# Kernel tuning notes

Hardware: AMD Instinct MI355X
Metric: run time of the kernel (lower is better)

The kernel has to match this reference:

```python
import jax, jax.numpy as jnp
import numpy as np

B, S, D, H, L, V = 2, 512, 1024, 16, 12, 50257
HD = D // H
DFF = 4 * D


def _ln(x, g, b, eps=1e-5):
    m = jnp.mean(x, axis=-1, keepdims=True)
    v = jnp.var(x, axis=-1, keepdims=True)
    return (x - m) * jax.lax.rsqrt(v + eps) * g + b


def setup_inputs() -> dict:
    key = jax.random.key(0)
    ks = jax.random.split(key, 32)
    sc = 0.02
    n = lambda k, shape: (jax.random.normal(k, shape, dtype=jnp.float32) * sc)
    inp = {
        "input_ids": jax.random.randint(ks[0], (B, S), 0, V, dtype=jnp.int64),
        "attention_mask": jnp.ones((B, S), dtype=jnp.float32),
        "image_hidden_states": jax.random.normal(ks[1], (B, D), dtype=jnp.float32),
        # token embedding table (also used for position embeds and tied lm_head, as in source)
        "wte": n(ks[2], (V, D)),
        # feature_space_transformation_nn: Linear(1024,1024) -> ReLU -> Linear(1024,1024)
        "ft_W1": n(ks[3], (D, D)), "ft_b1": jnp.zeros((D,), jnp.float32),
        "ft_W2": n(ks[4], (D, D)), "ft_b2": jnp.zeros((D,), jnp.float32),
        # per-layer params, stacked on leading L dim
        "ln1_g": jnp.ones((L, D), jnp.float32), "ln1_b": jnp.zeros((L, D), jnp.float32),
        "Wattn": n(ks[5], (L, D, 3 * D)), "battn": jnp.zeros((L, 3 * D), jnp.float32),
        "Wuk": n(ks[6], (L, D, D)), "buk": jnp.zeros((L, D), jnp.float32),
        "Wuv": n(ks[7], (L, D, D)), "buv": jnp.zeros((L, D), jnp.float32),
        "Wproj": n(ks[8], (L, D, D)), "bproj": jnp.zeros((L, D), jnp.float32),
        "ln2_g": jnp.ones((L, D), jnp.float32), "ln2_b": jnp.zeros((L, D), jnp.float32),
        "Wfc": n(ks[9], (L, D, DFF)), "bfc": jnp.zeros((L, DFF), jnp.float32),
        "Wfc2": n(ks[10], (L, DFF, D)), "bfc2": jnp.zeros((L, D), jnp.float32),
        "lnf_g": jnp.ones((D,), jnp.float32), "lnf_b": jnp.zeros((D,), jnp.float32),
    }
    return inp


def _forward(input_ids, attention_mask, image_hidden_states, wte,
             ft_W1, ft_b1, ft_W2, ft_b2,
             ln1_g, ln1_b, Wattn, battn, Wuk, buk, Wuv, buv, Wproj, bproj,
             ln2_g, ln2_b, Wfc, bfc, Wfc2, bfc2, lnf_g, lnf_b):
    # image feature transformation: Linear -> ReLU -> Linear
    img = jax.nn.relu(image_hidden_states @ ft_W1 + ft_b1) @ ft_W2 + ft_b2  # [B,D]

    # NOTE: source uses wte (not wpe) for position embeddings — faithful reproduction
    h = wte[input_ids] + wte[jnp.arange(S)][None]  # [B,S,D]

    # extended attention mask with a prepended zero column for the image token
    mask_ext = (1.0 - attention_mask)[:, None, None, :] * -10000.0  # [B,1,1,S]
    mask_ext = jnp.concatenate([jnp.zeros((B, 1, 1, 1), mask_ext.dtype), mask_ext], axis=-1)  # [B,1,1,S+1]

    # causal mask over kv_len=S+1: query i sees keys j <= i+1 (image token always visible)
    causal = jnp.arange(S + 1)[None, :] <= (jnp.arange(S)[:, None] + 1)  # [S,S+1]

    def block(h, p):
        (l1g, l1b, Wa, ba, Wk, bk, Wv, bv, Wp, bp, l2g, l2b, Wf, bf, Wf2, bf2) = p
        x = _ln(h, l1g, l1b)
        qkv = x @ Wa + ba
        q, k, v = jnp.split(qkv, 3, axis=-1)  # each [B,S,D]
        ki = (img @ Wk + bk)[:, None, :]  # [B,1,D]
        vi = (img @ Wv + bv)[:, None, :]
        k = jnp.concatenate([ki, k], axis=1)  # [B,S+1,D]
        v = jnp.concatenate([vi, v], axis=1)
        sh = lambda t, n: t.reshape(B, n, H, HD).transpose(0, 2, 1, 3)
        qh, kh, vh = sh(q, S), sh(k, S + 1), sh(v, S + 1)
        s = jnp.einsum('bhqd,bhkd->bhqk', qh, kh) / jnp.sqrt(jnp.float32(HD))
        s = jnp.where(causal[None, None], s, jnp.float32(-10000.0))
        s = s + mask_ext
        a = jax.nn.softmax(s, axis=-1)
        o = jnp.einsum('bhqk,bhkd->bhqd', a, vh).transpose(0, 2, 1, 3).reshape(B, S, D)
        h = h + (o @ Wp + bp)
        x = _ln(h, l2g, l2b)
        h = h + (jax.nn.gelu(x @ Wf + bf, approximate=True) @ Wf2 + bf2)
        return h, None

    params = (ln1_g, ln1_b, Wattn, battn, Wuk, buk, Wuv, buv, Wproj, bproj,
              ln2_g, ln2_b, Wfc, bfc, Wfc2, bfc2)
    h, _ = jax.lax.scan(block, h, params)
    h = _ln(h, lnf_g, lnf_b)
    return h @ wte.T  # tied lm head -> [B,S,V]


def reference(input_ids, attention_mask, image_hidden_states, wte,
              ft_W1, ft_b1, ft_W2, ft_b2,
              ln1_g, ln1_b, Wattn, battn, Wuk, buk, Wuv, buv, Wproj, bproj,
              ln2_g, ln2_b, Wfc, bfc, Wfc2, bfc2, lnf_g, lnf_b):
    return _forward(input_ids, attention_mask, image_hidden_states, wte,
                    ft_W1, ft_b1, ft_W2, ft_b2,
                    ln1_g, ln1_b, Wattn, battn, Wuk, buk, Wuv, buv, Wproj, bproj,
                    ln2_g, ln2_b, Wfc, bfc, Wfc2, bfc2, lnf_g, lnf_b)
```

## Files before the change

kernel.cpp:

```cpp
#include <hip/hip_runtime.h>
#include <cstdint>


typedef __bf16 bf16x8 __attribute__((ext_vector_type(8)));
typedef __bf16 bf16x4 __attribute__((ext_vector_type(4)));
typedef float  f32x4  __attribute__((ext_vector_type(4)));

#define GLDS16(g, l) __builtin_amdgcn_global_load_lds( \
    (const __attribute__((address_space(1))) unsigned int*)(g), \
    (__attribute__((address_space(3))) unsigned int*)(l), 16, 0, 0)

#define SCHED_FENCE() __builtin_amdgcn_sched_barrier(0)

__device__ __forceinline__ float gelu_f(float x) {
    float u = 1.5957691216057308f * (x + 0.044715f * x * x * x);
    float e = __expf(u);
    float t = 1.0f - 2.0f / (e + 1.0f);
    return 0.5f * x * (1.0f + t);
}

__device__ __forceinline__ int fragoff(int row, int kh, int hi) {
    return row * 64 + ((kh * 32 + hi * 8) ^ ((row & 7) << 3));
}

__device__ __forceinline__ void tcvt_body(
    int id, const float* __restrict__ Wa, const float* __restrict__ Wp,
    const float* __restrict__ Wf, const float* __restrict__ Wf2,
    __bf16* __restrict__ oa, __bf16* __restrict__ op,
    __bf16* __restrict__ of, __bf16* __restrict__ of2, float* tile)
{
    const float* src; __bf16* dst; int K, N, kb, nb;
    if (id < 768)       { src = Wa;  dst = oa;  K = 1024; N = 3072; kb = id & 15; nb = id >> 4; }
    else if (id < 1024) { id -= 768;  src = Wp;  dst = op;  K = 1024; N = 1024; kb = id & 15; nb = id >> 4; }
    else if (id < 2048) { id -= 1024; src = Wf;  dst = of;  K = 1024; N = 4096; kb = id & 15; nb = id >> 4; }
    else                { id -= 2048; src = Wf2; dst = of2; K = 4096; N = 1024; kb = id & 63; nb = id >> 6; }
    const int k0 = kb * 64, n0 = nb * 64;
    const int t = threadIdx.x;
    #pragma unroll
    for (int i = 0; i < 4; i++) {
        int r = i * 16 + (t >> 4), c = (t & 15) * 4;
        float4 v = *reinterpret_cast<const float4*>(src + (long)(k0 + r) * N + n0 + c);
        tile[r * 65 + c] = v.x; tile[r * 65 + c + 1] = v.y;
        tile[r * 65 + c + 2] = v.z; tile[r * 65 + c + 3] = v.w;
    }
    __syncthreads();
    const int nrow = t >> 2, kc = (t & 3) * 16;
    bf16x8 o0, o1;
    #pragma unroll
    for (int i = 0; i < 8; i++) {
        o0[i] = (__bf16)tile[(kc + i) * 65 + nrow];
        o1[i] = (__bf16)tile[(kc + 8 + i) * 65 + nrow];
    }
    *reinterpret_cast<bf16x8*>(dst + (long)(n0 + nrow) * K + k0 + kc)     = o0;
    *reinterpret_cast<bf16x8*>(dst + (long)(n0 + nrow) * K + k0 + kc + 8) = o1;
}

__device__ __forceinline__ void wcvt_body(
    int id, const float* __restrict__ wte, __bf16* __restrict__ out, long nvalid)
{
    long base = (long)id * 8192 + threadIdx.x * 8;
    #pragma unroll
    for (int i = 0; i < 4; i++) {
        long e = base + (long)i * 2048;
        bf16x8 o;
        if (e < nvalid) {
            float4 a = *reinterpret_cast<const float4*>(wte + e);
            float4 b = *reinterpret_cast<const float4*>(wte + e + 4);
            o[0] = (__bf16)a.x; o[1] = (__bf16)a.y; o[2] = (__bf16)a.z; o[3] = (__bf16)a.w;
            o[4] = (__bf16)b.x; o[5] = (__bf16)b.y; o[6] = (__bf16)b.z; o[7] = (__bf16)b.w;
        } else {
            #pragma unroll
            for (int q = 0; q < 8; q++) o[q] = (__bf16)0.f;
        }
        *reinterpret_cast<bf16x8*>(out + e) = o;
    }
}

__global__ __launch_bounds__(256) void tcvt_std(
    const float* __restrict__ Wa, const float* __restrict__ Wp,
    const float* __restrict__ Wf, const float* __restrict__ Wf2,
    __bf16* __restrict__ oa, __bf16* __restrict__ op,
    __bf16* __restrict__ of, __bf16* __restrict__ of2)
{
    __shared__ float tile[64 * 65];
    tcvt_body(blockIdx.x, Wa, Wp, Wf, Wf2, oa, op, of, of2, tile);
}

__global__ __launch_bounds__(256) void wcvt_std(
    const float* __restrict__ wte, __bf16* __restrict__ out, long nvalid)
{
    wcvt_body(blockIdx.x, wte, out, nvalid);
}

__global__ __launch_bounds__(256) void gemv_part(
    const float* __restrict__ x, int xld,
    const float* __restrict__ W, long wzs,
    float* __restrict__ part, int K, int N)
{
    int jb = blockIdx.x, kz = blockIdx.y, z = blockIdx.z;
    int t = threadIdx.x;
    int j = (jb << 6) + (t & 63);
    int g = t >> 6;
    int klen = K / (gridDim.y * 4);
    int kbase = (kz * 4 + g) * klen;
    const float* Wp = W + (long)z * wzs + (long)kbase * N + j;
    const float* x0 = x + kbase;
    const float* x1 = x + xld + kbase;
    float a0 = 0.f, a1 = 0.f;
    for (int k = 0; k < klen; k++) {
        float wv = Wp[(long)k * N];
        a0 += x0[k] * wv;
        a1 += x1[k] * wv;
    }
    __shared__ float r0[4][64], r1[4][64];
    r0[g][t & 63] = a0; r1[g][t & 63] = a1;
    __syncthreads();
    if (t < 64) {
        a0 = r0[0][t] + r0[1][t] + r0[2][t] + r0[3][t];
        a1 = r1[0][t] + r1[1][t] + r1[2][t] + r1[3][t];
        long base = (long)(z * gridDim.y + kz) * 2 * N + (jb << 6) + t;
        part[base]     = a0;
        part[base + N] = a1;
    }
}

__global__ __launch_bounds__(256) void gemv_reduce(
    const float* __restrict__ part, const float* __restrict__ bias, long bzs,
    float* __restrict__ out, int N, int nz, int act)
{
    int idx = blockIdx.x * 256 + threadIdx.x;
    if (idx >= nz * 2 * N) return;
    int j  = idx % N;
    int bz = idx / N;
    int z  = bz >> 1;
    float s = bias[(long)z * bzs + j];
    const float* p = part + ((long)z * 8 * 2 + (bz & 1)) * N + j;
    #pragma unroll
    for (int kz = 0; kz < 8; kz++) s += p[(long)kz * 2 * N];
    if (act) s = fmaxf(s, 0.f);
    out[idx] = s;
}

__global__ __launch_bounds__(256) void gemv_kv_part(
    const float* __restrict__ img,
    const float* __restrict__ Wuk, const float* __restrict__ Wuv,
    float* __restrict__ part)
{
    int jb = blockIdx.x, kz = blockIdx.y, z = blockIdx.z;
    int t = threadIdx.x;
    int j = (jb << 6) + (t & 63);
    int g = t >> 6;
    int kbase = (kz * 4 + g) * 64;
    const float* W = (z < 12) ? (Wuk + (long)z * 1048576) : (Wuv + (long)(z - 12) * 1048576);
    const float* Wp = W + (long)kbase * 1024 + j;
    const float* x0 = img + kbase;
    const float* x1 = img + 1024 + kbase;
    float a0 = 0.f, a1 = 0.f;
    for (int k = 0; k < 64; k++) {
        float wv = Wp[(long)k * 1024];
        a0 += x0[k] * wv;
        a1 += x1[k] * wv;
    }
    __shared__ float r0[4][64], r1[4][64];
    r0[g][t & 63] = a0; r1[g][t & 63] = a1;
    __syncthreads();
    if (t < 64) {
        a0 = r0[0][t] + r0[1][t] + r0[2][t] + r0[3][t];
        a1 = r1[0][t] + r1[1][t] + r1[2][t] + r1[3][t];
        long base = (long)(z * 4 + kz) * 2 * 1024 + (jb << 6) + t;
        part[base]        = a0;
        part[base + 1024] = a1;
    }
}

__global__ __launch_bounds__(256) void gemv_kv_reduce(
    const float* __restrict__ part,
    const float* __restrict__ buk, const float* __restrict__ buv,
    float* __restrict__ imgk, float* __restrict__ imgv)
{
    int idx = blockIdx.x * 256 + threadIdx.x;
    int z = idx >> 11;
    int bsel = (idx >> 10) & 1;
    int j = idx & 1023;
    float s = (z < 12) ? buk[z * 1024 + j] : buv[(z - 12) * 1024 + j];
    const float* p = part + ((long)z * 4 * 2 + bsel) * 1024 + j;
    #pragma unroll
    for (int kz = 0; kz < 4; kz++) s += p[(long)kz * 2 * 1024];
    if (z < 12) imgk[z * 2048 + bsel * 1024 + j] = s;
    else        imgv[(z - 12) * 2048 + bsel * 1024 + j] = s;
}

__global__ __launch_bounds__(256) void embed_ln(
    const int* __restrict__ ids, const float* __restrict__ wte,
    float* __restrict__ h, __bf16* __restrict__ xb,
    const float* __restrict__ g, const float* __restrict__ b)
{
    int row = blockIdx.x;
    int s = row & 511;
    int t = threadIdx.x;
    long id = ids[row];
    float4 v1 = reinterpret_cast<const float4*>(wte + id * 1024)[t];
    float4 v2 = reinterpret_cast<const float4*>(wte + (long)s * 1024)[t];
    float4 v; v.x = v1.x + v2.x; v.y = v1.y + v2.y; v.z = v1.z + v2.z; v.w = v1.w + v2.w;
    reinterpret_cast<float4*>(h + (long)row * 1024)[t] = v;

    float s1 = v.x + v.y + v.z + v.w;
    float s2 = v.x * v.x + v.y * v.y + v.z * v.z + v.w * v.w;
    #pragma unroll
    for (int o = 32; o >= 1; o >>= 1) { s1 += __shfl_xor(s1, o); s2 += __shfl_xor(s2, o); }
    __shared__ float r1[4], r2[4];
    int w = t >> 6;
    if ((t & 63) == 0) { r1[w] = s1; r2[w] = s2; }
    __syncthreads();
    s1 = r1[0] + r1[1] + r1[2] + r1[3];
    s2 = r2[0] + r2[1] + r2[2] + r2[3];
    float mean = s1 * (1.0f / 1024.0f);
    float var  = s2 * (1.0f / 1024.0f) - mean * mean;
    float rstd = rsqrtf(var + 1e-5f);
    float4 gg = reinterpret_cast<const float4*>(g)[t];
    float4 bb = reinterpret_cast<const float4*>(b)[t];
    bf16x4 o;
    o[0] = (__bf16)((v.x - mean) * rstd * gg.x + bb.x);
    o[1] = (__bf16)((v.y - mean) * rstd * gg.y + bb.y);
    o[2] = (__bf16)((v.z - mean) * rstd * gg.z + bb.z);
    o[3] = (__bf16)((v.w - mean) * rstd * gg.w + bb.w);
    *reinterpret_cast<bf16x4*>(xb + (long)row * 1024 + t * 4) = o;
}

__global__ __launch_bounds__(256) void ln_k(
    const float* __restrict__ in, __bf16* __restrict__ out,
    const float* __restrict__ g, const float* __restrict__ b)
{
    int row = blockIdx.x, t = threadIdx.x;
    float4 v = reinterpret_cast<const float4*>(in + (long)row * 1024)[t];
    float s1 = v.x + v.y + v.z + v.w;
    float s2 = v.x * v.x + v.y * v.y + v.z * v.z + v.w * v.w;
    #pragma unroll
    for (int o = 32; o >= 1; o >>= 1) { s1 += __shfl_xor(s1, o); s2 += __shfl_xor(s2, o); }
    __shared__ float r1[4], r2[4];
    int w = t >> 6;
    if ((t & 63) == 0) { r1[w] = s1; r2[w] = s2; }
    __syncthreads();
    s1 = r1[0] + r1[1] + r1[2] + r1[3];
    s2 = r2[0] + r2[1] + r2[2] + r2[3];
    float mean = s1 * (1.0f / 1024.0f);
    float var  = s2 * (1.0f / 1024.0f) - mean * mean;
    float rstd = rsqrtf(var + 1e-5f);
    float4 gg = reinterpret_cast<const float4*>(g)[t];
    float4 bb = reinterpret_cast<const float4*>(b)[t];
    bf16x4 o;
    o[0] = (__bf16)((v.x - mean) * rstd * gg.x + bb.x);
    o[1] = (__bf16)((v.y - mean) * rstd * gg.y + bb.y);
    o[2] = (__bf16)((v.z - mean) * rstd * gg.z + bb.z);
    o[3] = (__bf16)((v.w - mean) * rstd * gg.w + bb.w);
    *reinterpret_cast<bf16x4*>(out + (long)row * 1024 + t * 4) = o;
}

template<int NP>
__global__ __launch_bounds__(256) void lnadd_k(
    float* __restrict__ h, const float* __restrict__ part,
    const float* __restrict__ bias,
    const float* __restrict__ g, const float* __restrict__ b,
    __bf16* __restrict__ out)
{
    int row = blockIdx.x, t = threadIdx.x;
    long off = (long)row * 1024 + t * 4;
    float4 v = *reinterpret_cast<const float4*>(h + off);
    #pragma unroll
    for (int sp = 0; sp < NP; sp++) {
        float4 pv = *reinterpret_cast<const float4*>(part + sp * 1048576L + off);
        v.x += pv.x; v.y += pv.y; v.z += pv.z; v.w += pv.w;
    }
    float4 bi = reinterpret_cast<const float4*>(bias)[t];
    v.x += bi.x; v.y += bi.y; v.z += bi.z; v.w += bi.w;
    *reinterpret_cast<float4*>(h + off) = v;

    float s1 = v.x + v.y + v.z + v.w;
    float s2 = v.x * v.x + v.y * v.y + v.z * v.z + v.w * v.w;
    #pragma unroll
    for (int o = 32; o >= 1; o >>= 1) { s1 += __shfl_xor(s1, o); s2 += __shfl_xor(s2, o); }
    __shared__ float r1[4], r2[4];
    int w = t >> 6;
    if ((t & 63) == 0) { r1[w] = s1; r2[w] = s2; }
    __syncthreads();
    s1 = r1[0] + r1[1] + r1[2] + r1[3];
    s2 = r2[0] + r2[1] + r2[2] + r2[3];
    float mean = s1 * (1.0f / 1024.0f);
    float var  = s2 * (1.0f / 1024.0f) - mean * mean;
    float rstd = rsqrtf(var + 1e-5f);
    float4 gg = reinterpret_cast<const float4*>(g)[t];
    float4 bb = reinterpret_cast<const float4*>(b)[t];
    bf16x4 o;
    o[0] = (__bf16)((v.x - mean) * rstd * gg.x + bb.x);
    o[1] = (__bf16)((v.y - mean) * rstd * gg.y + bb.y);
    o[2] = (__bf16)((v.z - mean) * rstd * gg.z + bb.z);
    o[3] = (__bf16)((v.w - mean) * rstd * gg.w + bb.w);
    *reinterpret_cast<bf16x4*>(out + off) = o;
}

__global__ __launch_bounds__(512) void gemm256(
    const __bf16* __restrict__ A, const __bf16* __restrict__ Bt,
    float* __restrict__ C, int N, int K, int GM, int GN)
{
    const int total = GM * GN;
    const int q = total >> 3, r = total & 7;
    const int x = blockIdx.x & 7, jj = blockIdx.x >> 3;
    const int w0 = (x < r) ? x * (q + 1) + jj : r * (q + 1) + (x - r) * q + jj;
    const int m0 = (w0 % GM) * 256;
    const int n0 = (w0 / GM) * 256;

    __shared__ __bf16 As[2][256 * 64];
    __shared__ __bf16 Bs[2][256 * 64];
    const int t = threadIdx.x;
    const int wid = t >> 6, lane = t & 63;
    const int lo = lane & 15, hi = lane >> 4;
    const int wr = wid >> 2, wc = wid & 3;

    f32x4 acc[8][4] = {};

    const int srow = t >> 3;
    const int skx  = (((t & 7) ^ (srow & 7)) << 3);
    const int sldst = t * 8;
    #define ST256(bf, kk) do { \
        _Pragma("unroll") \
        for (int i = 0; i < 4; i++) \
            GLDS16(A + (long)(m0 + i * 64 + srow) * K + (kk) + skx, &As[bf][i * 4096 + sldst]); \
        _Pragma("unroll") \
        for (int i = 0; i < 4; i++) \
            GLDS16(Bt + (long)(n0 + i * 64 + srow) * K + (kk) + skx, &Bs[bf][i * 4096 + sldst]); \
    } while (0)

    const int T = K >> 6;
    ST256(0, 0);
    int cur = 0;
    for (int it = 0; it < T; it++) {
        if (it + 1 < T) {
            ST256(cur ^ 1, (it + 1) * 64);
            asm volatile("s_waitcnt vmcnt(8)" ::: "memory");
        } else {
            asm volatile("s_waitcnt vmcnt(0)" ::: "memory");
        }
        SCHED_FENCE();
        __builtin_amdgcn_s_barrier();
        SCHED_FENCE();

        #pragma unroll
        for (int kh = 0; kh < 2; kh++) {
            bf16x8 afr[8], bfr[4];
            #pragma unroll
            for (int mi = 0; mi < 8; mi++)
                afr[mi] = *reinterpret_cast<const bf16x8*>(&As[cur][fragoff(wr * 128 + mi * 16 + lo, kh, hi)]);
            #pragma unroll
            for (int ni = 0; ni < 4; ni++)
                bfr[ni] = *reinterpret_cast<const bf16x8*>(&Bs[cur][fragoff(wc * 64 + ni * 16 + lo, kh, hi)]);
            #pragma unroll
            for (int mi = 0; mi < 8; mi++)
                #pragma unroll
                for (int ni = 0; ni < 4; ni++)
                    acc[mi][ni] = __builtin_amdgcn_mfma_f32_16x16x32_bf16(afr[mi], bfr[ni], acc[mi][ni], 0, 0, 0);
        }

        SCHED_FENCE();
        __builtin_amdgcn_s_barrier();
        SCHED_FENCE();
        cur ^= 1;
    }
    #undef ST256

    #pragma unroll
    for (int mi = 0; mi < 8; mi++)
        #pragma unroll
        for (int ni = 0; ni < 4; ni++) {
            int col = n0 + wc * 64 + ni * 16 + lo;
            if (col >= N) continue;
            #pragma unroll
            for (int rr = 0; rr < 4; rr++) {
                int row = m0 + wr * 128 + mi * 16 + hi * 4 + rr;
                C[(long)row * N + col] = acc[mi][ni][rr];
            }
        }
}

template<int BN, int OUTBF16, int ACT, int PARTIAL>
__global__ __launch_bounds__(256) void gemm64(
    const __bf16* __restrict__ A, const __bf16* __restrict__ Bt,
    const float* __restrict__ bias, void* __restrict__ C,
    int N, int K, int GM, int GN, int NS)
{
    constexpr int NB = BN / 32;
    const int total = GM * GN * NS;
    const int q = total >> 3, r = total & 7;
    const int x = blockIdx.x & 7, jj = blockIdx.x >> 3;
    const int w0 = (x < r) ? x * (q + 1) + jj : r * (q + 1) + (x - r) * q + jj;
    const int sp = w0 / (GM * GN);
    const int rem = w0 - sp * (GM * GN);
    const int m0 = (rem % GM) * 64;
    const int n0 = (rem / GM) * BN;

    __shared__ __bf16 As[2][64 * 64];
    __shared__ __bf16 Bs[2][BN * 64];
    const int t = threadIdx.x;
    const int wv = t >> 6, lane = t & 63;
    const int lo = lane & 15, hi = lane >> 4;
    const int wr = wv >> 1, wc = wv & 1;

    f32x4 acc[2][NB] = {};

    const int srow = t >> 3;
    const int skx  = (((t & 7) ^ (srow & 7)) << 3);
    const int sldst = t * 8;
    #define ST64(bf, kk) do { \
        _Pragma("unroll") \
        for (int i = 0; i < 2; i++) \
            GLDS16(A + (long)(m0 + i * 32 + srow) * K + (kk) + skx, &As[bf][i * 2048 + sldst]); \
        _Pragma("unroll") \
        for (int i = 0; i < NB; i++) \
            GLDS16(Bt + (long)(n0 + i * 32 + srow) * K + (kk) + skx, &Bs[bf][i * 2048 + sldst]); \
    } while (0)

    const int Ksp = K / NS;
    const int kbeg = sp * Ksp;
    const int T = Ksp >> 6;

    ST64(0, kbeg);
    int cur = 0;
    for (int it = 0; it < T; it++) {
        if (it + 1 < T) {
            ST64(cur ^ 1, kbeg + (it + 1) * 64);
            if constexpr (NB == 4) asm volatile("s_waitcnt vmcnt(6)" ::: "memory");
            else                   asm volatile("s_waitcnt vmcnt(4)" ::: "memory");
        } else {
            asm volatile("s_waitcnt vmcnt(0)" ::: "memory");
        }
        SCHED_FENCE();
        __builtin_amdgcn_s_barrier();
        SCHED_FENCE();

        #pragma unroll
        for (int kh = 0; kh < 2; kh++) {
            bf16x8 afr[2], bfr[NB];
            #pragma unroll
            for (int mi = 0; mi < 2; mi++)
                afr[mi] = *reinterpret_cast<const bf16x8*>(&As[cur][fragoff(wr * 32 + mi * 16 + lo, kh, hi)]);
            #pragma unroll
            for (int ni = 0; ni < NB; ni++)
                bfr[ni] = *reinterpret_cast<const bf16x8*>(&Bs[cur][fragoff(wc * (BN / 2) + ni * 16 + lo, kh, hi)]);
            #pragma unroll
            for (int mi = 0; mi < 2; mi++)
                #pragma unroll
                for (int ni = 0; ni < NB; ni++)
                    acc[mi][ni] = __builtin_amdgcn_mfma_f32_16x16x32_bf16(afr[mi], bfr[ni], acc[mi][ni], 0, 0, 0);
        }

        SCHED_FENCE();
        __builtin_amdgcn_s_barrier();
        SCHED_FENCE();
        cur ^= 1;
    }
    #undef ST64

    const long coff = PARTIAL ? (long)sp * GM * 64 * N : 0;
    #pragma unroll
    for (int mi = 0; mi < 2; mi++)
        #pragma unroll
        for (int ni = 0; ni < NB; ni++) {
            int col = n0 + wc * (BN / 2) + ni * 16 + lo;
            float bv = (!PARTIAL && bias) ? bias[col] : 0.f;
            #pragma unroll
            for (int rr = 0; rr < 4; rr++) {
                int row = m0 + wr * 32 + mi * 16 + hi * 4 + rr;
                float v = acc[mi][ni][rr] + bv;
                if (ACT) v = gelu_f(v);
                if (OUTBF16) ((__bf16*)C)[(long)row * N + col] = (__bf16)v;
                else         ((float*)C)[coff + (long)row * N + col] = v;
            }
        }
}

template<int OUTBF16, int ACT, int RES>
__global__ __launch_bounds__(256) void gemm_bb(
    const __bf16* __restrict__ A, const __bf16* __restrict__ Bt,
    const float* __restrict__ bias, const float* __restrict__ res,
    void* __restrict__ C, int N, int K)
{
    __shared__ __bf16 As[64 * 32];
    __shared__ __bf16 Bs[64 * 32];
    const int t = threadIdx.x;
    const int m0 = blockIdx.x * 64;
    const int n0 = blockIdx.y * 64;
    const int w = t >> 6, lane = t & 63;
    const int lo = lane & 15, hi = lane >> 4;
    const int wr = w >> 1, wc = w & 1;

    f32x4 acc[2][2] = {};

    for (int k0 = 0; k0 < K; k0 += 32) {
        __syncthreads();
        GLDS16(A  + (long)(m0 + (t >> 2)) * K + k0 + ((t & 3) << 3), &As[t * 8]);
        GLDS16(Bt + (long)(n0 + (t >> 2)) * K + k0 + ((t & 3) << 3), &Bs[t * 8]);
        __syncthreads();
        bf16x8 afr[2], bfr[2];
        #pragma unroll
        for (int mi = 0; mi < 2; mi++)
            afr[mi] = *reinterpret_cast<const bf16x8*>(&As[(wr * 32 + mi * 16 + lo) * 32 + hi * 8]);
        #pragma unroll
        for (int ni = 0; ni < 2; ni++)
            bfr[ni] = *reinterpret_cast<const bf16x8*>(&Bs[(wc * 32 + ni * 16 + lo) * 32 + hi * 8]);
        #pragma unroll
        for (int mi = 0; mi < 2; mi++)
            #pragma unroll
            for (int ni = 0; ni < 2; ni++)
                acc[mi][ni] = __builtin_amdgcn_mfma_f32_16x16x32_bf16(afr[mi], bfr[ni], acc[mi][ni], 0, 0, 0);
    }

    #pragma unroll
    for (int mi = 0; mi < 2; mi++)
        #pragma unroll
        for (int ni = 0; ni < 2; ni++) {
            int col = n0 + wc * 32 + ni * 16 + lo;
            float bv = bias ? bias[col] : 0.f;
            #pragma unroll
            for (int rr = 0; rr < 4; rr++) {
                int row = m0 + wr * 32 + mi * 16 + hi * 4 + rr;
                float v = acc[mi][ni][rr] + bv;
                if (ACT) v = gelu_f(v);
                if (RES) v += res[(long)row * N + col];
                if (OUTBF16) ((__bf16*)C)[(long)row * N + col] = (__bf16)v;
                else         ((float*)C)[(long)row * N + col] = v;
            }
        }
}

__global__ __launch_bounds__(256) void gemm_lm(
    const __bf16* __restrict__ A, const float* __restrict__ Wt,
    float* __restrict__ C, int N, int K)
{
    __shared__ __bf16 As[128 * 32];
    __shared__ __bf16 Bs[128 * 32];
    const int t = threadIdx.x;
    const int m0 = blockIdx.x * 128;
    const int n0 = blockIdx.y * 128;
    const int w = t >> 6, lane = t & 63;
    const int lo = lane & 15, hi = lane >> 4;
    const int wr = w >> 1, wc = w & 1;

    f32x4 acc[4][4] = {};

    for (int k0 = 0; k0 < K; k0 += 32) {
        __syncthreads();
        #pragma unroll
        for (int i = 0; i < 2; i++) {
            int c = i * 256 + t;
            GLDS16(A + (long)(m0 + (c >> 2)) * K + k0 + ((c & 3) << 3), &As[c * 8]);
        }
        #pragma unroll
        for (int i = 0; i < 2; i++) {
            int c = i * 256 + t;
            int nr = n0 + (c >> 2);
            bf16x8 bv;
            if (nr < N) {
                const float* wp = Wt + (long)nr * K + k0 + ((c & 3) << 3);
                float4 b0 = *reinterpret_cast<const float4*>(wp);
                float4 b1 = *reinterpret_cast<const float4*>(wp + 4);
                bv[0] = (__bf16)b0.x; bv[1] = (__bf16)b0.y; bv[2] = (__bf16)b0.z; bv[3] = (__bf16)b0.w;
                bv[4] = (__bf16)b1.x; bv[5] = (__bf16)b1.y; bv[6] = (__bf16)b1.z; bv[7] = (__bf16)b1.w;
            } else {
                #pragma unroll
                for (int qq = 0; qq < 8; qq++) bv[qq] = (__bf16)0.f;
            }
            *reinterpret_cast<bf16x8*>(&Bs[c * 8]) = bv;
        }
        __syncthreads();
        bf16x8 afr[4], bfr[4];
        #pragma unroll
        for (int mi = 0; mi < 4; mi++)
            afr[mi] = *reinterpret_cast<const bf16x8*>(&As[(wr * 64 + mi * 16 + lo) * 32 + hi * 8]);
        #pragma unroll
        for (int ni = 0; ni < 4; ni++)
            bfr[ni] = *reinterpret_cast<const bf16x8*>(&Bs[(wc * 64 + ni * 16 + lo) * 32 + hi * 8]);
        #pragma unroll
        for (int mi = 0; mi < 4; mi++)
            #pragma unroll
            for (int ni = 0; ni < 4; ni++)
                acc[mi][ni] = __builtin_amdgcn_mfma_f32_16x16x32_bf16(afr[mi], bfr[ni], acc[mi][ni], 0, 0, 0);
    }

    #pragma unroll
    for (int mi = 0; mi < 4; mi++)
        #pragma unroll
        for (int ni = 0; ni < 4; ni++) {
            int col = n0 + wc * 64 + ni * 16 + lo;
            if (col < N) {
                #pragma unroll
                for (int rr = 0; rr < 4; rr++) {
                    int row = m0 + wr * 64 + mi * 16 + hi * 4 + rr;
                    C[(long)row * N + col] = acc[mi][ni][rr];
                }
            }
        }
}

__global__ __launch_bounds__(256) void attn_aux(
    const __bf16* __restrict__ qkv,
    const float* __restrict__ imgk, const float* __restrict__ imgv,
    const float* __restrict__ amask, __bf16* __restrict__ out,
    int aux_mode,
    const float* __restrict__ Wa, const float* __restrict__ Wp,
    const float* __restrict__ Wf, const float* __restrict__ Wf2,
    __bf16* __restrict__ oa, __bf16* __restrict__ op,
    __bf16* __restrict__ of, __bf16* __restrict__ of2,
    const float* __restrict__ wte, __bf16* __restrict__ wteb, long nvalid)
{
    __shared__ __align__(16) char smem[28416];
    const int bid = blockIdx.x;
    if (bid >= 256) {
        if (aux_mode == 1)
            tcvt_body(bid - 256, Wa, Wp, Wf, Wf2, oa, op, of, of2, (float*)smem);
        else
            wcvt_body(bid - 256, wte, wteb, nvalid);
        return;
    }

    __bf16 (*Ks)[72] = (__bf16(*)[72])(smem);
    __bf16 (*Vt)[72] = (__bf16(*)[72])(smem + 9216);
    __bf16 (*Ps)[16][72] = (__bf16(*)[16][72])(smem + 18432);
    float* kimg_s = (float*)(smem + 27648);
    float* amv_s  = (float*)(smem + 27904);

    const int qb = bid & 7;
    const int h  = (bid >> 3) & 15;
    const int b  = bid >> 7;
    const int t = threadIdx.x, w = t >> 6, lane = t & 63;
    const int lo = lane & 15, hi = lane >> 4;

    const int kr8 = t >> 2, kd8 = (t & 3) * 16;
    const int vr8 = t & 63, vd8 = (t >> 6) * 16;

    const __bf16* qrow = qkv + (long)(b * 512 + qb * 64 + w * 16 + lo) * 3072 + h * 64;
    bf16x8 qf0 = *reinterpret_cast<const bf16x8*>(qrow + hi * 8);
    bf16x8 qf1 = *reinterpret_cast<const bf16x8*>(qrow + 32 + hi * 8);

    if (t < 64) kimg_s[t] = imgk[b * 1024 + h * 64 + t];
    __syncthreads();

    float simg = 0.f;
    #pragma unroll
    for (int i = 0; i < 8; i++)
        simg += (float)qf0[i] * kimg_s[hi * 8 + i] + (float)qf1[i] * kimg_s[32 + hi * 8 + i];
    simg += __shfl_xor(simg, 16);
    simg += __shfl_xor(simg, 32);
    simg *= 0.125f;

    float pimg[4], l_part[4];
    f32x4 o_acc[4];
    #pragma unroll
    for (int rr = 0; rr < 4; rr++) {
        pimg[rr] = __expf(__shfl(simg, hi * 4 + rr));
        l_part[rr] = 0.f;
    }
    #pragma unroll
    for (int df = 0; df < 4; df++) {
        float vi = imgv[b * 1024 + h * 64 + df * 16 + lo];
        #pragma unroll
        for (int rr = 0; rr < 4; rr++) o_acc[df][rr] = pimg[rr] * vi;
    }

    bf16x8 ck0, ck1, cv0, cv1;
    {
        const __bf16* ks = qkv + (long)(b * 512 + kr8) * 3072 + 1024 + h * 64 + kd8;
        ck0 = *reinterpret_cast<const bf16x8*>(ks);
        ck1 = *reinterpret_cast<const bf16x8*>(ks + 8);
        const __bf16* vs = qkv + (long)(b * 512 + vr8) * 3072 + 2048 + h * 64 + vd8;
        cv0 = *reinterpret_cast<const bf16x8*>(vs);
        cv1 = *reinterpret_cast<const bf16x8*>(vs + 8);
    }

    for (int kb = 0; kb <= qb; kb++) {
        bf16x8 nk0, nk1, nv0, nv1;
        const bool more = (kb < qb);
        if (more) {
            const __bf16* ks = qkv + (long)(b * 512 + (kb + 1) * 64 + kr8) * 3072 + 1024 + h * 64 + kd8;
            nk0 = *reinterpret_cast<const bf16x8*>(ks);
            nk1 = *reinterpret_cast<const bf16x8*>(ks + 8);
            const __bf16* vs = qkv + (long)(b * 512 + (kb + 1) * 64 + vr8) * 3072 + 2048 + h * 64 + vd8;
            nv0 = *reinterpret_cast<const bf16x8*>(vs);
            nv1 = *reinterpret_cast<const bf16x8*>(vs + 8);
        }
        __syncthreads();
        *reinterpret_cast<bf16x8*>(&Ks[kr8][kd8])     = ck0;
        *reinterpret_cast<bf16x8*>(&Ks[kr8][kd8 + 8]) = ck1;
        #pragma unroll
        for (int i = 0; i < 8; i++) { Vt[vd8 + i][vr8] = cv0[i]; Vt[vd8 + 8 + i][vr8] = cv1[i]; }
        if (t < 64) amv_s[t] = (1.0f - amask[b * 512 + kb * 64 + t]) * -10000.0f;
        __syncthreads();

        f32x4 sf[4];
        #pragma unroll
        for (int js = 0; js < 4; js++) {
            bf16x8 kf0 = *reinterpret_cast<const bf16x8*>(&Ks[js * 16 + lo][hi * 8]);
            bf16x8 kf1 = *reinterpret_cast<const bf16x8*>(&Ks[js * 16 + lo][32 + hi * 8]);
            f32x4 a = {};
            a = __builtin_amdgcn_mfma_f32_16x16x32_bf16(qf0, kf0, a, 0, 0, 0);
            a = __builtin_amdgcn_mfma_f32_16x16x32_bf16(qf1, kf1, a, 0, 0, 0);
            sf[js] = a;
        }
        #pragma unroll
        for (int js = 0; js < 4; js++) {
            float amv = amv_s[js * 16 + lo];
            #pragma unroll
            for (int rr = 0; rr < 4; rr++) {
                float sv = sf[js][rr] * 0.125f + amv;
                if (kb == qb) {
                    int qrw = w * 16 + hi * 4 + rr;
                    if (js * 16 + lo > qrw) sv = -10000.0f + amv;
                }
                float p = __expf(sv);
                l_part[rr] += p;
                Ps[w][hi * 4 + rr][js * 16 + lo] = (__bf16)p;
            }
        }
        #pragma unroll
        for (int jb = 0; jb < 2; jb++) {
            bf16x8 pf = *reinterpret_cast<const bf16x8*>(&Ps[w][lo][jb * 32 + hi * 8]);
            #pragma unroll
            for (int df = 0; df < 4; df++) {
                bf16x8 vf = *reinterpret_cast<const bf16x8*>(&Vt[df * 16 + lo][jb * 32 + hi * 8]);
                o_acc[df] = __builtin_amdgcn_mfma_f32_16x16x32_bf16(pf, vf, o_acc[df], 0, 0, 0);
            }
        }
        if (more) { ck0 = nk0; ck1 = nk1; cv0 = nv0; cv1 = nv1; }
    }

    float linv[4];
    #pragma unroll
    for (int rr = 0; rr < 4; rr++) {
        float ls = l_part[rr];
        #pragma unroll
        for (int off = 1; off < 16; off <<= 1) ls += __shfl_xor(ls, off);
        linv[rr] = 1.0f / (pimg[rr] + ls);
    }
    #pragma unroll
    for (int df = 0; df < 4; df++)
        #pragma unroll
        for (int rr = 0; rr < 4; rr++) {
            long row = b * 512 + qb * 64 + w * 16 + hi * 4 + rr;
            out[row * 1024 + h * 64 + df * 16 + lo] = (__bf16)(o_acc[df][rr] * linv[rr]);
        }
}

extern "C" void kernel_launch(void* const* d_in, const int* in_sizes, int n_in,
                              void* d_out, int out_size, void* d_ws, size_t ws_size,
                              hipStream_t stream) {
    (void)in_sizes; (void)n_in; (void)out_size;
    const int*   ids   = (const int*)d_in[0];
    const float* amask = (const float*)d_in[1];
    const float* ihs   = (const float*)d_in[2];
    const float* wte   = (const float*)d_in[3];
    const float* ftW1  = (const float*)d_in[4];
    const float* ftb1  = (const float*)d_in[5];
    const float* ftW2  = (const float*)d_in[6];
    const float* ftb2  = (const float*)d_in[7];
    const float* ln1g  = (const float*)d_in[8];
    const float* ln1b  = (const float*)d_in[9];
    const float* Wattn = (const float*)d_in[10];
    const float* battn = (const float*)d_in[11];
    const float* Wuk   = (const float*)d_in[12];
    const float* buk   = (const float*)d_in[13];
    const float* Wuv   = (const float*)d_in[14];
    const float* buv   = (const float*)d_in[15];
    const float* Wproj = (const float*)d_in[16];
    const float* bproj = (const float*)d_in[17];
    const float* ln2g  = (const float*)d_in[18];
    const float* ln2b  = (const float*)d_in[19];
    const float* Wfc   = (const float*)d_in[20];
    const float* bfc   = (const float*)d_in[21];
    const float* Wfc2  = (const float*)d_in[22];
    const float* bfc2  = (const float*)d_in[23];
    const float* lnfg  = (const float*)d_in[24];
    const float* lnfb  = (const float*)d_in[25];
    float* out = (float*)d_out;

    const long VP2 = 50432;
    const long NVALID = 50257L * 1024;
    char* base = (char*)d_ws;
    float* ftmp  = (float*)(base);
    float* img   = (float*)(base + (1 << 13));
    float* imgk  = (float*)(base + (1 << 14));
    float* imgv  = (float*)(base + 114688);
    float* part  = (float*)(base + 212992);
    float* h     = (float*)(base + 1048576);
    char* p = base + 5 * 1048576;
    __bf16* xb    = (__bf16*)p; p += 2 * 1048576;
    __bf16* qkvb  = (__bf16*)p; p += 6 * 1048576;
    __bf16* attob = (__bf16*)p; p += 2 * 1048576;
    __bf16* ffb   = (__bf16*)p; p += 8 * 1048576;
    __bf16* wtA0  = (__bf16*)p; p += 6 * 1048576;
    __bf16* wtP0  = (__bf16*)p; p += 2 * 1048576;
    __bf16* wtF0  = (__bf16*)p; p += 8 * 1048576;
    __bf16* wtF20 = (__bf16*)p; p += 8 * 1048576;
    __bf16* wteb  = (__bf16*)p; p += VP2 * 1024 * 2;
    size_t need1 = (size_t)(p - base);
    float* part_g = (float*)(base + need1);
    size_t need2 = need1 + 4 * 1048576 * sizeof(float);
    char* p2 = base + need2;
    __bf16* wtA1  = (__bf16*)p2; p2 += 6 * 1048576;
    __bf16* wtP1  = (__bf16*)p2; p2 += 2 * 1048576;
    __bf16* wtF1  = (__bf16*)p2; p2 += 8 * 1048576;
    __bf16* wtF21 = (__bf16*)p2; p2 += 8 * 1048576;
    size_t need3 = (size_t)(p2 - base);
    const bool big1 = (ws_size >= need1);
    const bool big2 = (ws_size >= need2);
    const bool big3 = (ws_size >= need3);

    __bf16* wtA_s[2]  = {wtA0, wtA1};
    __bf16* wtP_s[2]  = {wtP0, wtP1};
    __bf16* wtF_s[2]  = {wtF0, wtF1};
    __bf16* wtF2_s[2] = {wtF20, wtF21};

    dim3 b256(256);

    gemv_part<<<dim3(16, 8, 1), b256, 0, stream>>>(ihs, 1024, ftW1, 0, part, 1024, 1024);
    gemv_reduce<<<dim3(8), b256, 0, stream>>>(part, ftb1, 0, ftmp, 1024, 1, 1);
    gemv_part<<<dim3(16, 8, 1), b256, 0, stream>>>(ftmp, 1024, ftW2, 0, part, 1024, 1024);
    gemv_reduce<<<dim3(8), b256, 0, stream>>>(part, ftb2, 0, img, 1024, 1, 0);
    gemv_kv_part<<<dim3(16, 4, 24), b256, 0, stream>>>(img, Wuk, Wuv, part);
    gemv_kv_reduce<<<dim3(192), b256, 0, stream>>>(part, buk, buv, imgk, imgv);

    embed_ln<<<dim3(1024), b256, 0, stream>>>(ids, wte, h, xb, ln1g, ln1b);
    tcvt_std<<<dim3(3072), b256, 0, stream>>>(
        Wattn, Wproj, Wfc, Wfc2, wtA0, wtP0, wtF0, wtF20);

    for (int l = 0; l < 12; l++) {
        const int cs = big3 ? (l & 1) : 0;
        __bf16* cA  = wtA_s[cs];
        __bf16* cP  = wtP_s[cs];
        __bf16* cF  = wtF_s[cs];
        __bf16* cF2 = wtF2_s[cs];

        if (!big3 && l > 0) {
            tcvt_std<<<dim3(3072), b256, 0, stream>>>(
                Wattn + (long)l * 1024 * 3072, Wproj + (long)l * 1024 * 1024,
                Wfc + (long)l * 1024 * 4096, Wfc2 + (long)l * 4096 * 1024,
                wtA0, wtP0, wtF0, wtF20);
        }

        gemm64<128, 1, 0, 0><<<dim3(384), b256, 0, stream>>>(
            xb, cA, battn + l * 3072, qkvb, 3072, 1024, 16, 24, 1);

        if (big3 && l < 11) {
            const int ns = (l + 1) & 1;
            attn_aux<<<dim3(256 + 3072), b256, 0, stream>>>(
                qkvb, imgk + l * 2048, imgv + l * 2048, amask, attob, 1,
                Wattn + (long)(l + 1) * 1024 * 3072, Wproj + (long)(l + 1) * 1024 * 1024,
                Wfc + (long)(l + 1) * 1024 * 4096, Wfc2 + (long)(l + 1) * 4096 * 1024,
                wtA_s[ns], wtP_s[ns], wtF_s[ns], wtF2_s[ns],
                nullptr, nullptr, 0);
        } else if (big3 && l == 11) {
            attn_aux<<<dim3(256 + 6304), b256, 0, stream>>>(
                qkvb, imgk + l * 2048, imgv + l * 2048, amask, attob, 2,
                nullptr, nullptr, nullptr, nullptr,
                nullptr, nullptr, nullptr, nullptr,
                wte, wteb, NVALID);
        } else {
            attn_aux<<<dim3(256), b256, 0, stream>>>(
                qkvb, imgk + l * 2048, imgv + l * 2048, amask, attob, 0,
                nullptr, nullptr, nullptr, nullptr,
                nullptr, nullptr, nullptr, nullptr,
                nullptr, nullptr, 0);
        }

        const float* ng = (l < 11) ? (ln1g + (l + 1) * 1024) : lnfg;
        const float* nb = (l < 11) ? (ln1b + (l + 1) * 1024) : lnfb;
        if (big2) {
            gemm64<64, 0, 0, 1><<<dim3(512), b256, 0, stream>>>(
                attob, cP, nullptr, part_g, 1024, 1024, 16, 16, 2);
            lnadd_k<2><<<dim3(1024), b256, 0, stream>>>(
                h, part_g, bproj + l * 1024, ln2g + l * 1024, ln2b + l * 1024, xb);
            gemm64<128, 1, 1, 0><<<dim3(512), b256, 0, stream>>>(
                xb, cF, bfc + l * 4096, ffb, 4096, 1024, 16, 32, 1);
            gemm64<128, 0, 0, 1><<<dim3(512), b256, 0, stream>>>(
                ffb, cF2, nullptr, part_g, 1024, 4096, 16, 8, 4);
            lnadd_k<4><<<dim3(1024), b256, 0, stream>>>(
                h, part_g, bfc2 + l * 1024, ng, nb, xb);
        } else {
            gemm_bb<0, 0, 1><<<dim3(16, 16), b256, 0, stream>>>(
                attob, cP, bproj + l * 1024, h, h, 1024, 1024);
            ln_k<<<dim3(1024), b256, 0, stream>>>(h, xb, ln2g + l * 1024, ln2b + l * 1024);
            gemm64<128, 1, 1, 0><<<dim3(512), b256, 0, stream>>>(
                xb, cF, bfc + l * 4096, ffb, 4096, 1024, 16, 32, 1);
            gemm_bb<0, 0, 1><<<dim3(16, 16), b256, 0, stream>>>(
                ffb, cF2, bfc2 + l * 1024, h, h, 1024, 4096);
            ln_k<<<dim3(1024), b256, 0, stream>>>(h, xb, ng, nb);
        }
    }

    if (big1) {
        if (!big3)
            wcvt_std<<<dim3((unsigned)(VP2 * 1024 / 8192)), b256, 0, stream>>>(wte, wteb, NVALID);
        gemm256<<<dim3(788), dim3(512), 0, stream>>>(
            xb, wteb, out, 50257, 1024, 4, (int)(VP2 / 256));
    } else {
        gemm_lm<<<dim3(8, 393), b256, 0, stream>>>(xb, wte, out, 50257, 1024);
    }
}
```

Measured before the change: 1.474 ms.

## Retile LM-head GEMM to 128x256 tiles with K=32 stages for occupancy

```diff
diff --git a/kernel.cpp b/kernel.cpp
--- a/kernel.cpp
+++ b/kernel.cpp
@@ -21,6 +21,9 @@
 
 __device__ __forceinline__ int fragoff(int row, int kh, int hi) {
     return row * 64 + ((kh * 32 + hi * 8) ^ ((row & 7) << 3));
+}
+__device__ __forceinline__ int fragoff32(int row, int hi) {
+    return row * 32 + ((hi * 8) ^ ((row & 3) << 3));
 }
 
 __device__ __forceinline__ void tcvt_body(
@@ -298,7 +301,7 @@
     *reinterpret_cast<bf16x4*>(out + off) = o;
 }
 
-__global__ __launch_bounds__(512) void gemm256(
+__global__ __launch_bounds__(512, 4) void gemm_lm2(
     const __bf16* __restrict__ A, const __bf16* __restrict__ Bt,
     float* __restrict__ C, int N, int K, int GM, int GN)
 {
@@ -306,37 +309,34 @@
     const int q = total >> 3, r = total & 7;
     const int x = blockIdx.x & 7, jj = blockIdx.x >> 3;
     const int w0 = (x < r) ? x * (q + 1) + jj : r * (q + 1) + (x - r) * q + jj;
-    const int m0 = (w0 % GM) * 256;
+    const int m0 = (w0 % GM) * 128;
     const int n0 = (w0 / GM) * 256;
 
-    __shared__ __bf16 As[2][256 * 64];
-    __shared__ __bf16 Bs[2][256 * 64];
+    __shared__ __bf16 As[2][128 * 32];
+    __shared__ __bf16 Bs[2][256 * 32];
     const int t = threadIdx.x;
     const int wid = t >> 6, lane = t & 63;
     const int lo = lane & 15, hi = lane >> 4;
     const int wr = wid >> 2, wc = wid & 3;
 
-    f32x4 acc[8][4] = {};
-
-    const int srow = t >> 3;
-    const int skx  = (((t & 7) ^ (srow & 7)) << 3);
+    f32x4 acc[4][4] = {};
+
+    const int srow = t >> 2;
+    const int skx  = (((t & 3) ^ (srow & 3)) << 3);
     const int sldst = t * 8;
-    #define ST256(bf, kk) do { \
-        _Pragma("unroll") \
-        for (int i = 0; i < 4; i++) \
-            GLDS16(A + (long)(m0 + i * 64 + srow) * K + (kk) + skx, &As[bf][i * 4096 + sldst]); \
-        _Pragma("unroll") \
-        for (int i = 0; i < 4; i++) \
-            GLDS16(Bt + (long)(n0 + i * 64 + srow) * K + (kk) + skx, &Bs[bf][i * 4096 + sldst]); \
+    #define STLM(bf, kk) do { \
+        GLDS16(A + (long)(m0 + srow) * K + (kk) + skx, &As[bf][sldst]); \
+        GLDS16(Bt + (long)(n0 + srow)       * K + (kk) + skx, &Bs[bf][sldst]); \
+        GLDS16(Bt + (long)(n0 + 128 + srow) * K + (kk) + skx, &Bs[bf][4096 + sldst]); \
     } while (0)
 
-    const int T = K >> 6;
-    ST256(0, 0);
+    const int T = K >> 5;
+    STLM(0, 0);
     int cur = 0;
     for (int it = 0; it < T; it++) {
         if (it + 1 < T) {
-            ST256(cur ^ 1, (it + 1) * 64);
-            asm volatile("s_waitcnt vmcnt(8)" ::: "memory");
+            STLM(cur ^ 1, (it + 1) * 32);
+            asm volatile("s_waitcnt vmcnt(3)" ::: "memory");
         } else {
             asm volatile("s_waitcnt vmcnt(0)" ::: "memory");
         }
@@ -344,38 +344,37 @@
         __builtin_amdgcn_s_barrier();
         SCHED_FENCE();
 
-        #pragma unroll
-        for (int kh = 0; kh < 2; kh++) {
-            bf16x8 afr[8], bfr[4];
-            #pragma unroll
-            for (int mi = 0; mi < 8; mi++)
-                afr[mi] = *reinterpret_cast<const bf16x8*>(&As[cur][fragoff(wr * 128 + mi * 16 + lo, kh, hi)]);
+        bf16x8 afr[4], bfr[4];
+        #pragma unroll
+        for (int mi = 0; mi < 4; mi++)
+            afr[mi] = *reinterpret_cast<const bf16x8*>(&As[cur][fragoff32(wr * 64 + mi * 16 + lo, hi)]);
+        #pragma unroll
+        for (int ni = 0; ni < 4; ni++)
+            bfr[ni] = *reinterpret_cast<const bf16x8*>(&Bs[cur][fragoff32(wc * 64 + ni * 16 + lo, hi)]);
+        __builtin_amdgcn_s_setprio(1);
+        #pragma unroll
+        for (int mi = 0; mi < 4; mi++)
             #pragma unroll
             for (int ni = 0; ni < 4; ni++)
-                bfr[ni] = *reinterpret_cast<const bf16x8*>(&Bs[cur][fragoff(wc * 64 + ni * 16 + lo, kh, hi)]);
-            #pragma unroll
-            for (int mi = 0; mi < 8; mi++)
-                #pragma unroll
-                for (int ni = 0; ni < 4; ni++)
-                    acc[mi][ni] = __builtin_amdgcn_mfma_f32_16x16x32_bf16(afr[mi], bfr[ni], acc[mi][ni], 0, 0, 0);
-        }
+                acc[mi][ni] = __builtin_amdgcn_mfma_f32_16x16x32_bf16(afr[mi], bfr[ni], acc[mi][ni], 0, 0, 0);
+        __builtin_amdgcn_s_setprio(0);
 
         SCHED_FENCE();
         __builtin_amdgcn_s_barrier();
         SCHED_FENCE();
         cur ^= 1;
     }
-    #undef ST256
-
-    #pragma unroll
-    for (int mi = 0; mi < 8; mi++)
+    #undef STLM
+
+    #pragma unroll
+    for (int mi = 0; mi < 4; mi++)
         #pragma unroll
         for (int ni = 0; ni < 4; ni++) {
             int col = n0 + wc * 64 + ni * 16 + lo;
             if (col >= N) continue;
             #pragma unroll
             for (int rr = 0; rr < 4; rr++) {
-                int row = m0 + wr * 128 + mi * 16 + hi * 4 + rr;
+                int row = m0 + wr * 64 + mi * 16 + hi * 4 + rr;
                 C[(long)row * N + col] = acc[mi][ni][rr];
             }
         }
@@ -445,11 +444,13 @@
             #pragma unroll
             for (int ni = 0; ni < NB; ni++)
                 bfr[ni] = *reinterpret_cast<const bf16x8*>(&Bs[cur][fragoff(wc * (BN / 2) + ni * 16 + lo, kh, hi)]);
+            __builtin_amdgcn_s_setprio(1);
             #pragma unroll
             for (int mi = 0; mi < 2; mi++)
                 #pragma unroll
                 for (int ni = 0; ni < NB; ni++)
                     acc[mi][ni] = __builtin_amdgcn_mfma_f32_16x16x32_bf16(afr[mi], bfr[ni], acc[mi][ni], 0, 0, 0);
+            __builtin_amdgcn_s_setprio(0);
         }
 
         SCHED_FENCE();
@@ -897,8 +898,8 @@
     if (big1) {
         if (!big3)
             wcvt_std<<<dim3((unsigned)(VP2 * 1024 / 8192)), b256, 0, stream>>>(wte, wteb, NVALID);
-        gemm256<<<dim3(788), dim3(512), 0, stream>>>(
-            xb, wteb, out, 50257, 1024, 4, (int)(VP2 / 256));
+        gemm_lm2<<<dim3(8 * (int)(VP2 / 256)), dim3(512), 0, stream>>>(
+            xb, wteb, out, 50257, 1024, 8, (int)(VP2 / 256));
     } else {
         gemm_lm<<<dim3(8, 393), b256, 0, stream>>>(xb, wte, out, 50257, 1024);
     }
```

Result: no change. 1.477 ms (+0.2%).
